# Kernel optimization log

Hardware: AMD Instinct MI355X
Metric: run time of the kernel (lower is better)

## Reference

```python
import jax, jax.numpy as jnp
import numpy as np

DIM = 256
BETA = 4
B, L, L1 = 16, 2048, 4096
EPS = 1e-6


def setup_inputs() -> dict:
    key = jax.random.key(0)
    ks = jax.random.split(key, 20)
    d, db = DIM, DIM // BETA
    s = lambda *sh: 0.02
    inp = {
        "features": jax.random.normal(ks[0], (B, L, d), jnp.float32),
        "quires_box": jax.random.uniform(ks[1], (B, L1, 2), jnp.float32),
        "quires_features": jax.random.normal(ks[2], (B, L1, d), jnp.float32),
        "pos_feature": jax.random.normal(ks[3], (B, L1, d), jnp.float32),
        # contrast1 params
        "c1_w1": jax.random.normal(ks[4], (db, d), jnp.float32) * 0.02,
        "c1_b1": jnp.zeros((db,), jnp.float32),
        "c1_w2": jax.random.normal(ks[5], (d, db), jnp.float32) * 0.02,
        "c1_b2": jnp.zeros((d,), jnp.float32),
        "c1_g": jnp.ones((d,), jnp.float32),
        "c1_be": jnp.zeros((d,), jnp.float32),
        # contrast2 params
        "c2_w1": jax.random.normal(ks[6], (db, d), jnp.float32) * 0.02,
        "c2_b1": jnp.zeros((db,), jnp.float32),
        "c2_w2": jax.random.normal(ks[7], (d, db), jnp.float32) * 0.02,
        "c2_b2": jnp.zeros((d,), jnp.float32),
        "c2_g": jnp.ones((d,), jnp.float32),
        "c2_be": jnp.zeros((d,), jnp.float32),
        # gate MLP (Prediction: Linear(2d->d)+ReLU+Linear(d->2), dropout=identity at eval)
        "g_w1": jax.random.normal(ks[8], (d, 2 * d), jnp.float32) * 0.02,
        "g_b1": jnp.zeros((d,), jnp.float32),
        "g_w2": jax.random.normal(ks[9], (2, d), jnp.float32) * 0.02,
        "g_b2": jnp.zeros((2,), jnp.float32),
    }
    return inp


def _contrast(v1, v2, w1, b1, w2, b2, g, be):
    # v1, v2: [B, N, C]. Pointwise conv1 -> ReLU -> conv2 -> LayerNorm -> sigmoid -> *v1
    v = v1 * v2
    h = jax.nn.relu(jnp.einsum('bnc,dc->bnd', v, w1) + b1)  # [B,N,C/beta]
    u = jnp.einsum('bnd,cd->bnc', h, w2) + b2               # [B,N,C]
    mu = jnp.mean(u, axis=-1, keepdims=True)
    var = jnp.mean(jnp.square(u - mu), axis=-1, keepdims=True)
    ln = (u - mu) * jax.lax.rsqrt(var + EPS) * g + be
    return jax.nn.sigmoid(ln) * v1


def reference(features, quires_box, quires_features, pos_feature,
              c1_w1, c1_b1, c1_w2, c1_b2, c1_g, c1_be,
              c2_w1, c2_b1, c2_w2, c2_b2, c2_g, c2_be,
              g_w1, g_b1, g_w2, g_b2):
    Lf = features.shape[1]
    cx, w = quires_box[..., 0], quires_box[..., 1]
    roi_start = jnp.round(jnp.clip((cx - w / 2) * Lf, 0, Lf - 1)).astype(jnp.int32)
    roi_end = jnp.round(jnp.clip((cx + w / 2) * Lf, 0, Lf - 1)).astype(jnp.int32)
    sf = jnp.take_along_axis(features, roi_start[..., None], axis=1)  # [B,L1,C]
    ef = jnp.take_along_axis(features, roi_end[..., None], axis=1)    # [B,L1,C]
    sf = _contrast(sf, pos_feature, c1_w1, c1_b1, c1_w2, c1_b2, c1_g, c1_be)
    ef = _contrast(ef, pos_feature, c2_w1, c2_b1, c2_w2, c2_b2, c2_g, c2_be)
    pooled = (sf + ef) * 0.5  # aligned_len=True -> mean over the 2 boundaries
    x = jnp.concatenate([pooled, quires_features], axis=-1)  # [B,L1,2C]
    h = jax.nn.relu(jnp.einsum('bnc,dc->bnd', x, g_w1) + g_b1)
    gate = jax.nn.softmax(jnp.einsum('bnd,od->bno', h, g_w2) + g_b2, axis=-1)
    out = pooled * gate[..., 0:1] + quires_features * gate[..., 1:2]
    return jnp.swapaxes(out, 0, 1)  # [L1, B, C]
```

## Files before the change

kernel.cpp:

```cpp
#include <hip/hip_runtime.h>
#include <hip/hip_bf16.h>
#include <math.h>

typedef __attribute__((ext_vector_type(8))) short bf16x8;
typedef __attribute__((ext_vector_type(4))) float f32x4;
typedef __attribute__((ext_vector_type(2))) __fp16 f16x2;
typedef __attribute__((ext_vector_type(4))) unsigned int u32x4;
typedef __attribute__((ext_vector_type(2))) unsigned int u32x2;

constexpr int NB = 16, NQ = 4096, LF = 2048, C = 256;

__device__ __forceinline__ unsigned short bfbits(float x) {
    return __builtin_bit_cast(unsigned short, __float2bfloat16(x));
}
__device__ __forceinline__ unsigned pk2(float a, float b) {
    return (unsigned)bfbits(a) | ((unsigned)bfbits(b) << 16);
}
__device__ __forceinline__ float bflo(unsigned d) { return __builtin_bit_cast(float, d << 16); }
__device__ __forceinline__ float bfhi(unsigned d) { return __builtin_bit_cast(float, d & 0xffff0000u); }
__device__ __forceinline__ unsigned pkh(float a, float b) {
    f16x2 h = __builtin_amdgcn_cvt_pkrtz(a, b);
    return __builtin_bit_cast(unsigned, h);
}
__device__ __forceinline__ float hlo(unsigned u) {
    f16x2 h = __builtin_bit_cast(f16x2, u); return (float)h[0];
}
__device__ __forceinline__ float hhi(unsigned u) {
    f16x2 h = __builtin_bit_cast(f16x2, u); return (float)h[1];
}

__global__ void prep_weights(const float* __restrict__ c1w1, const float* __restrict__ c2w1,
                             const float* __restrict__ c1w2, const float* __restrict__ c2w2,
                             const float* __restrict__ gw1, unsigned short* __restrict__ ws)
{
    int t = blockIdx.x * 256 + threadIdx.x;
    const float* src; int K, nks, dstoff, f;
    if (t < 2048)      { src = c1w1; K = 256; nks = 8;  dstoff = 0;      f = t; }
    else if (t < 4096) { src = c2w1; K = 256; nks = 8;  dstoff = 16384;  f = t - 2048; }
    else if (t < 6144) { src = c1w2; K = 64;  nks = 2;  dstoff = 32768;  f = t - 4096; }
    else if (t < 8192) { src = c2w2; K = 64;  nks = 2;  dstoff = 49152;  f = t - 6144; }
    else               { src = gw1;  K = 512; nks = 16; dstoff = 65536;  f = t - 8192; }
    int l = f & 63, s = f >> 6;
    int nt = s / nks, ks = s % nks;
    int n  = nt * 16 + (l & 15);
    int k0 = ks * 32 + (l >> 4) * 8;
    unsigned short* d = ws + dstoff + (size_t)f * 8;
    const float* sp = src + (size_t)n * K + k0;
    #pragma unroll
    for (int e = 0; e < 8; ++e) d[e] = bfbits(sp[e]);
}

__global__ __launch_bounds__(256, 4)
void semalign_v17(const float* __restrict__ feat,  const float* __restrict__ qbox,
                  const float* __restrict__ qfeat, const float* __restrict__ posf,
                  const float* __restrict__ c1b1,  const float* __restrict__ c1b2,
                  const float* __restrict__ c1g,   const float* __restrict__ c1be,
                  const float* __restrict__ c2b1,  const float* __restrict__ c2b2,
                  const float* __restrict__ c2g,   const float* __restrict__ c2be,
                  const float* __restrict__ gb1,   const float* __restrict__ gw2,
                  const float* __restrict__ gb2,
                  const unsigned short* __restrict__ wsb,
                  float* __restrict__ out)
{
    __shared__ __align__(16) unsigned short sP[4][16][256];

    const int tid = threadIdx.x, l = tid & 63, wid = tid >> 6;
    const int lr = l & 15, lg = l >> 4;
    const int rowb = blockIdx.x * 64 + wid * 16;
    const int q = rowb >> 4;
    const int b = lr;
    const int swz = (lr & 7) << 4;

    const float* prow = posf  + ((size_t)b * NQ + q) * C;
    const float* qrow = qfeat + ((size_t)b * NQ + q) * C;
    float cx = qbox[((size_t)b * NQ + q) * 2 + 0];
    float w  = qbox[((size_t)b * NQ + q) * 2 + 1];
    float fs = fminf(fmaxf((cx - 0.5f * w) * (float)LF, 0.f), (float)(LF - 1));
    float fe = fminf(fmaxf((cx + 0.5f * w) * (float)LF, 0.f), (float)(LF - 1));
    const float* srow = feat + ((size_t)b * LF + (int)rintf(fs)) * C;
    const float* erow = feat + ((size_t)b * LF + (int)rintf(fe)) * C;

    char* pb = (char*)&sP[wid][0][0];
    {
        f32x4 a1[4] = {}, a2[4] = {};
        #pragma unroll
        for (int ks = 0; ks < 8; ++ks) {
            int k0 = ks * 32 + lg * 8;
            float4 s0 = *(const float4*)(srow + k0), s1 = *(const float4*)(srow + k0 + 4);
            float4 e0 = *(const float4*)(erow + k0), e1 = *(const float4*)(erow + k0 + 4);
            float4 p0 = *(const float4*)(prow + k0), p1 = *(const float4*)(prow + k0 + 4);
            u32x4 av, cv;
            av[0] = pk2(s0.x * p0.x, s0.y * p0.y); av[1] = pk2(s0.z * p0.z, s0.w * p0.w);
            av[2] = pk2(s1.x * p1.x, s1.y * p1.y); av[3] = pk2(s1.z * p1.z, s1.w * p1.w);
            cv[0] = pk2(e0.x * p0.x, e0.y * p0.y); cv[1] = pk2(e0.z * p0.z, e0.w * p0.w);
            cv[2] = pk2(e1.x * p1.x, e1.y * p1.y); cv[3] = pk2(e1.z * p1.z, e1.w * p1.w);
            bf16x8 v1 = __builtin_bit_cast(bf16x8, av);
            bf16x8 v2 = __builtin_bit_cast(bf16x8, cv);
            #pragma unroll
            for (int nt = 0; nt < 4; ++nt) {
                bf16x8 wA = *(const bf16x8*)(wsb + ((size_t)((nt * 8 + ks) * 64 + l)) * 8);
                bf16x8 wB = *(const bf16x8*)(wsb + 16384 + ((size_t)((nt * 8 + ks) * 64 + l)) * 8);
                a1[nt] = __builtin_amdgcn_mfma_f32_16x16x32_bf16(wA, v1, a1[nt], 0, 0, 0);
                a2[nt] = __builtin_amdgcn_mfma_f32_16x16x32_bf16(wB, v2, a2[nt], 0, 0, 0);
            }
        }
        #pragma unroll
        for (int nt = 0; nt < 4; ++nt) {
            float4 b1v = *(const float4*)(c1b1 + nt * 16 + lg * 4);
            float4 b2v = *(const float4*)(c2b1 + nt * 16 + lg * 4);
            u32x2 wv;
            wv[0] = pk2(fmaxf(a1[nt][0] + b1v.x, 0.f), fmaxf(a1[nt][1] + b1v.y, 0.f));
            wv[1] = pk2(fmaxf(a1[nt][2] + b1v.z, 0.f), fmaxf(a1[nt][3] + b1v.w, 0.f));
            *(u32x2*)(pb + lr * 128 + ((nt * 32 + lg * 8) ^ swz)) = wv;
            wv[0] = pk2(fmaxf(a2[nt][0] + b2v.x, 0.f), fmaxf(a2[nt][1] + b2v.y, 0.f));
            wv[1] = pk2(fmaxf(a2[nt][2] + b2v.z, 0.f), fmaxf(a2[nt][3] + b2v.w, 0.f));
            *(u32x2*)(pb + 2048 + lr * 128 + ((nt * 32 + lg * 8) ^ swz)) = wv;
        }
    }

    f16x2 Ph[16][2];
    #pragma unroll
    for (int j = 0; j < 2; ++j) {
        char* hb = pb + j * 2048;
        asm volatile("s_waitcnt lgkmcnt(0)" ::: "memory");
        bf16x8 hf0 = *(const bf16x8*)(hb + lr * 128 + ((0 + lg * 16) ^ swz));
        bf16x8 hf1 = *(const bf16x8*)(hb + lr * 128 + ((64 + lg * 16) ^ swz));
        const unsigned short* w2b = wsb + (j ? 49152 : 32768);
        const float* b2p = j ? c2b2 : c1b2;
        const float* gp  = j ? c2g  : c1g;
        const float* bep = j ? c2be : c1be;
        const float* xrow = j ? erow : srow;
        float S = 0.f, Q2 = 0.f;

        {
            f32x4 u8[8] = {};
            #pragma unroll
            for (int nt = 0; nt < 8; ++nt) {
                bf16x8 wA = *(const bf16x8*)(w2b + ((size_t)((nt * 2 + 0) * 64 + l)) * 8);
                bf16x8 wB = *(const bf16x8*)(w2b + ((size_t)((nt * 2 + 1) * 64 + l)) * 8);
                u8[nt] = __builtin_amdgcn_mfma_f32_16x16x32_bf16(wA, hf0, u8[nt], 0, 0, 0);
                u8[nt] = __builtin_amdgcn_mfma_f32_16x16x32_bf16(wB, hf1, u8[nt], 0, 0, 0);
            }
            #pragma unroll
            for (int nt = 0; nt < 8; ++nt) {
                float4 bv = *(const float4*)(b2p + nt * 16 + lg * 4);
                u8[nt][0] += bv.x; u8[nt][1] += bv.y; u8[nt][2] += bv.z; u8[nt][3] += bv.w;
                S  += u8[nt][0] + u8[nt][1] + u8[nt][2] + u8[nt][3];
                Q2 += u8[nt][0] * u8[nt][0] + u8[nt][1] * u8[nt][1]
                    + u8[nt][2] * u8[nt][2] + u8[nt][3] * u8[nt][3];
                u32x2 wv;
                wv[0] = pkh(u8[nt][0], u8[nt][1]);
                wv[1] = pkh(u8[nt][2], u8[nt][3]);
                *(u32x2*)(pb + 4096 + nt * 512 + l * 8) = wv;
            }
        }
        f32x4 u8b[8] = {};
        #pragma unroll
        for (int nt = 0; nt < 8; ++nt) {
            bf16x8 wA = *(const bf16x8*)(w2b + ((size_t)(((nt + 8) * 2 + 0) * 64 + l)) * 8);
            bf16x8 wB = *(const bf16x8*)(w2b + ((size_t)(((nt + 8) * 2 + 1) * 64 + l)) * 8);
            u8b[nt] = __builtin_amdgcn_mfma_f32_16x16x32_bf16(wA, hf0, u8b[nt], 0, 0, 0);
            u8b[nt] = __builtin_amdgcn_mfma_f32_16x16x32_bf16(wB, hf1, u8b[nt], 0, 0, 0);
        }
        #pragma unroll
        for (int nt = 0; nt < 8; ++nt) {
            float4 bv = *(const float4*)(b2p + (nt + 8) * 16 + lg * 4);
            u8b[nt][0] += bv.x; u8b[nt][1] += bv.y; u8b[nt][2] += bv.z; u8b[nt][3] += bv.w;
            S  += u8b[nt][0] + u8b[nt][1] + u8b[nt][2] + u8b[nt][3];
            Q2 += u8b[nt][0] * u8b[nt][0] + u8b[nt][1] * u8b[nt][1]
                + u8b[nt][2] * u8b[nt][2] + u8b[nt][3] * u8b[nt][3];
        }
        S  += __shfl_xor(S, 16);  S  += __shfl_xor(S, 32);
        Q2 += __shfl_xor(Q2, 16); Q2 += __shfl_xor(Q2, 32);
        float mu  = S * (1.f / 256.f);
        float rsg = rsqrtf(Q2 * (1.f / 256.f) - mu * mu + 1e-6f);

        u32x2 st[8];
        asm volatile("s_waitcnt lgkmcnt(0)" ::: "memory");
        #pragma unroll
        for (int nt = 0; nt < 8; ++nt)
            st[nt] = *(const u32x2*)(pb + 4096 + nt * 512 + l * 8);
        asm volatile("s_waitcnt lgkmcnt(0)" ::: "memory");

        #pragma unroll
        for (int nt = 0; nt < 16; ++nt) {
            float u4[4];
            if (nt < 8) {
                u4[0] = hlo(st[nt][0]); u4[1] = hhi(st[nt][0]);
                u4[2] = hlo(st[nt][1]); u4[3] = hhi(st[nt][1]);
            } else {
                u4[0] = u8b[nt - 8][0]; u4[1] = u8b[nt - 8][1];
                u4[2] = u8b[nt - 8][2]; u4[3] = u8b[nt - 8][3];
            }
            float4 gv  = *(const float4*)(gp  + nt * 16 + lg * 4);
            float4 bev = *(const float4*)(bep + nt * 16 + lg * 4);
            float4 xv  = *(const float4*)(xrow + nt * 16 + lg * 4);
            float g4[4] = { gv.x, gv.y, gv.z, gv.w };
            float e4[4] = { bev.x, bev.y, bev.z, bev.w };
            float x4[4] = { xv.x, xv.y, xv.z, xv.w };
            float tm[4];
            #pragma unroll
            for (int r = 0; r < 4; ++r) {
                float ln = (u4[r] - mu) * rsg * g4[r] + e4[r];
                float sg = 1.f / (1.f + __expf(-ln));
                tm[r] = 0.5f * sg * x4[r];
            }
            if (j == 0) {
                Ph[nt][0] = __builtin_amdgcn_cvt_pkrtz(tm[0], tm[1]);
                Ph[nt][1] = __builtin_amdgcn_cvt_pkrtz(tm[2], tm[3]);
            } else {
                float p0 = (float)Ph[nt][0][0] + tm[0];
                float p1 = (float)Ph[nt][0][1] + tm[1];
                float p2 = (float)Ph[nt][1][0] + tm[2];
                float p3 = (float)Ph[nt][1][1] + tm[3];
                u32x2 wv;
                wv[0] = pk2(p0, p1); wv[1] = pk2(p2, p3);
                *(u32x2*)(pb + lr * 512 + ((nt * 32 + lg * 8) ^ swz)) = wv;
            }
        }
    }
    asm volatile("s_waitcnt lgkmcnt(0)" ::: "memory");

    f32x4 ga[16] = {};
    const unsigned short* gwb = wsb + 65536;
    #pragma clang loop unroll(disable)
    for (int kk = 0; kk < 16; ++kk) {
        bf16x8 xk;
        if (kk < 8) {
            xk = *(const bf16x8*)(pb + lr * 512 + ((kk * 64 + lg * 16) ^ swz));
        } else {
            int k0 = (kk - 8) * 32 + lg * 8;
            float4 q0 = *(const float4*)(qrow + k0), q1 = *(const float4*)(qrow + k0 + 4);
            u32x4 a;
            a[0] = pk2(q0.x, q0.y); a[1] = pk2(q0.z, q0.w);
            a[2] = pk2(q1.x, q1.y); a[3] = pk2(q1.z, q1.w);
            xk = __builtin_bit_cast(bf16x8, a);
        }
        #pragma unroll
        for (int nt = 0; nt < 16; ++nt) {
            bf16x8 wf = *(const bf16x8*)(gwb + ((size_t)((nt * 16 + kk) * 64 + l)) * 8);
            ga[nt] = __builtin_amdgcn_mfma_f32_16x16x32_bf16(wf, xk, ga[nt], 0, 0, 0);
        }
    }

    float t0 = 0.f, t1 = 0.f;
    #pragma unroll
    for (int nt = 0; nt < 16; ++nt) {
        float4 gbv = *(const float4*)(gb1 + nt * 16 + lg * 4);
        float4 w0v = *(const float4*)(gw2 + nt * 16 + lg * 4);
        float4 w1v = *(const float4*)(gw2 + 256 + nt * 16 + lg * 4);
        float gb4[4] = { gbv.x, gbv.y, gbv.z, gbv.w };
        float w04[4] = { w0v.x, w0v.y, w0v.z, w0v.w };
        float w14[4] = { w1v.x, w1v.y, w1v.z, w1v.w };
        #pragma unroll
        for (int r = 0; r < 4; ++r) {
            float hv = fmaxf(ga[nt][r] + gb4[r], 0.f);
            t0 += hv * w04[r]; t1 += hv * w14[r];
        }
    }
    t0 += __shfl_xor(t0, 16); t0 += __shfl_xor(t0, 32);
    t1 += __shfl_xor(t1, 16); t1 += __shfl_xor(t1, 32);
    float g0 = 1.f / (1.f + __expf((t1 + gb2[1]) - (t0 + gb2[0])));
    float g1 = 1.f - g0;

    float* orow = out + (size_t)(rowb + lr) * C;
    #pragma unroll
    for (int ks = 0; ks < 8; ++ks) {
        bf16x8 pf = *(const bf16x8*)(pb + lr * 512 + ((ks * 64 + lg * 16) ^ swz));
        u32x4 pu = __builtin_bit_cast(u32x4, pf);
        int k0 = ks * 32 + lg * 8;
        float4 q0 = *(const float4*)(qrow + k0), q1 = *(const float4*)(qrow + k0 + 4);
        float4 o0, o1;
        o0.x = bflo(pu[0]) * g0 + q0.x * g1;
        o0.y = bfhi(pu[0]) * g0 + q0.y * g1;
        o0.z = bflo(pu[1]) * g0 + q0.z * g1;
        o0.w = bfhi(pu[1]) * g0 + q0.w * g1;
        o1.x = bflo(pu[2]) * g0 + q1.x * g1;
        o1.y = bfhi(pu[2]) * g0 + q1.y * g1;
        o1.z = bflo(pu[3]) * g0 + q1.z * g1;
        o1.w = bfhi(pu[3]) * g0 + q1.w * g1;
        *(float4*)(orow + ks * 32 + lg * 8)     = o0;
        *(float4*)(orow + ks * 32 + lg * 8 + 4) = o1;
    }
}

extern "C" void kernel_launch(void* const* d_in, const int* in_sizes, int n_in,
                              void* d_out, int out_size, void* d_ws, size_t ws_size,
                              hipStream_t stream) {
    const float* feat  = (const float*)d_in[0];
    const float* qbox  = (const float*)d_in[1];
    const float* qfeat = (const float*)d_in[2];
    const float* posf  = (const float*)d_in[3];
    const float* c1w1  = (const float*)d_in[4];
    const float* c1b1  = (const float*)d_in[5];
    const float* c1w2  = (const float*)d_in[6];
    const float* c1b2  = (const float*)d_in[7];
    const float* c1g   = (const float*)d_in[8];
    const float* c1be  = (const float*)d_in[9];
    const float* c2w1  = (const float*)d_in[10];
    const float* c2b1  = (const float*)d_in[11];
    const float* c2w2  = (const float*)d_in[12];
    const float* c2b2  = (const float*)d_in[13];
    const float* c2g   = (const float*)d_in[14];
    const float* c2be  = (const float*)d_in[15];
    const float* gw1   = (const float*)d_in[16];
    const float* gb1   = (const float*)d_in[17];
    const float* gw2   = (const float*)d_in[18];
    const float* gb2   = (const float*)d_in[19];
    float* out = (float*)d_out;
    unsigned short* wsb = (unsigned short*)d_ws;

    prep_weights<<<96, 256, 0, stream>>>(c1w1, c2w1, c1w2, c2w2, gw1, wsb);

    dim3 grid((NB * NQ) / 64), block(256);
    semalign_v17<<<grid, block, 0, stream>>>(
        feat, qbox, qfeat, posf,
        c1b1, c1b2, c1g, c1be,
        c2b1, c2b2, c2g, c2be,
        gb1, gw2, gb2, wsb, out);
}
```

Measured before the change: 162.8 us.

## Recompute second-layer contrast MFMAs instead of staging u through LDS and registers

```diff
diff --git a/kernel.cpp b/kernel.cpp
--- a/kernel.cpp
+++ b/kernel.cpp
@@ -4,7 +4,6 @@
 
 typedef __attribute__((ext_vector_type(8))) short bf16x8;
 typedef __attribute__((ext_vector_type(4))) float f32x4;
-typedef __attribute__((ext_vector_type(2))) __fp16 f16x2;
 typedef __attribute__((ext_vector_type(4))) unsigned int u32x4;
 typedef __attribute__((ext_vector_type(2))) unsigned int u32x2;
 
@@ -18,16 +17,6 @@
 }
 __device__ __forceinline__ float bflo(unsigned d) { return __builtin_bit_cast(float, d << 16); }
 __device__ __forceinline__ float bfhi(unsigned d) { return __builtin_bit_cast(float, d & 0xffff0000u); }
-__device__ __forceinline__ unsigned pkh(float a, float b) {
-    f16x2 h = __builtin_amdgcn_cvt_pkrtz(a, b);
-    return __builtin_bit_cast(unsigned, h);
-}
-__device__ __forceinline__ float hlo(unsigned u) {
-    f16x2 h = __builtin_bit_cast(f16x2, u); return (float)h[0];
-}
-__device__ __forceinline__ float hhi(unsigned u) {
-    f16x2 h = __builtin_bit_cast(f16x2, u); return (float)h[1];
-}
 
 __global__ void prep_weights(const float* __restrict__ c1w1, const float* __restrict__ c2w1,
                              const float* __restrict__ c1w2, const float* __restrict__ c2w2,
@@ -51,7 +40,7 @@
 }
 
 __global__ __launch_bounds__(256, 4)
-void semalign_v17(const float* __restrict__ feat,  const float* __restrict__ qbox,
+void semalign_v18(const float* __restrict__ feat,  const float* __restrict__ qbox,
                   const float* __restrict__ qfeat, const float* __restrict__ posf,
                   const float* __restrict__ c1b1,  const float* __restrict__ c1b2,
                   const float* __restrict__ c1g,   const float* __restrict__ c1be,
@@ -118,105 +107,92 @@
         }
     }
 
-    f16x2 Ph[16][2];
+    asm volatile("s_waitcnt lgkmcnt(0)" ::: "memory");
+    bf16x8 hfA0 = *(const bf16x8*)(pb + lr * 128 + ((0  + lg * 16) ^ swz));
+    bf16x8 hfA1 = *(const bf16x8*)(pb + lr * 128 + ((64 + lg * 16) ^ swz));
+    bf16x8 hfB0 = *(const bf16x8*)(pb + 2048 + lr * 128 + ((0  + lg * 16) ^ swz));
+    bf16x8 hfB1 = *(const bf16x8*)(pb + 2048 + lr * 128 + ((64 + lg * 16) ^ swz));
+    asm volatile("s_waitcnt lgkmcnt(0)" ::: "memory");
+
+    float S1 = 0.f, Q21 = 0.f, S2 = 0.f, Q22 = 0.f;
     #pragma unroll
     for (int j = 0; j < 2; ++j) {
-        char* hb = pb + j * 2048;
-        asm volatile("s_waitcnt lgkmcnt(0)" ::: "memory");
-        bf16x8 hf0 = *(const bf16x8*)(hb + lr * 128 + ((0 + lg * 16) ^ swz));
-        bf16x8 hf1 = *(const bf16x8*)(hb + lr * 128 + ((64 + lg * 16) ^ swz));
         const unsigned short* w2b = wsb + (j ? 49152 : 32768);
         const float* b2p = j ? c2b2 : c1b2;
-        const float* gp  = j ? c2g  : c1g;
-        const float* bep = j ? c2be : c1be;
-        const float* xrow = j ? erow : srow;
+        bf16x8 h0 = j ? hfB0 : hfA0, h1 = j ? hfB1 : hfA1;
         float S = 0.f, Q2 = 0.f;
-
+        #pragma unroll
+        for (int nt = 0; nt < 16; ++nt) {
+            f32x4 u = {};
+            bf16x8 wA = *(const bf16x8*)(w2b + ((size_t)((nt * 2 + 0) * 64 + l)) * 8);
+            bf16x8 wB = *(const bf16x8*)(w2b + ((size_t)((nt * 2 + 1) * 64 + l)) * 8);
+            u = __builtin_amdgcn_mfma_f32_16x16x32_bf16(wA, h0, u, 0, 0, 0);
+            u = __builtin_amdgcn_mfma_f32_16x16x32_bf16(wB, h1, u, 0, 0, 0);
+            float4 bv = *(const float4*)(b2p + nt * 16 + lg * 4);
+            float b4[4] = { bv.x, bv.y, bv.z, bv.w };
+            #pragma unroll
+            for (int r = 0; r < 4; ++r) {
+                float v = u[r] + b4[r];
+                S += v; Q2 += v * v;
+            }
+        }
+        if (j == 0) { S1 = S; Q21 = Q2; } else { S2 = S; Q22 = Q2; }
+    }
+    S1 += __shfl_xor(S1, 16); S1 += __shfl_xor(S1, 32);
+    Q21 += __shfl_xor(Q21, 16); Q21 += __shfl_xor(Q21, 32);
+    S2 += __shfl_xor(S2, 16); S2 += __shfl_xor(S2, 32);
+    Q22 += __shfl_xor(Q22, 16); Q22 += __shfl_xor(Q22, 32);
+    float mu1 = S1 * (1.f / 256.f), rs1 = rsqrtf(Q21 * (1.f / 256.f) - mu1 * mu1 + 1e-6f);
+    float mu2 = S2 * (1.f / 256.f), rs2 = rsqrtf(Q22 * (1.f / 256.f) - mu2 * mu2 + 1e-6f);
+
+    #pragma unroll
+    for (int nt = 0; nt < 16; ++nt) {
+        float tm[4];
         {
-            f32x4 u8[8] = {};
-            #pragma unroll
-            for (int nt = 0; nt < 8; ++nt) {
-                bf16x8 wA = *(const bf16x8*)(w2b + ((size_t)((nt * 2 + 0) * 64 + l)) * 8);
-                bf16x8 wB = *(const bf16x8*)(w2b + ((size_t)((nt * 2 + 1) * 64 + l)) * 8);
-                u8[nt] = __builtin_amdgcn_mfma_f32_16x16x32_bf16(wA, hf0, u8[nt], 0, 0, 0);
-                u8[nt] = __builtin_amdgcn_mfma_f32_16x16x32_bf16(wB, hf1, u8[nt], 0, 0, 0);
-            }
-            #pragma unroll
-            for (int nt = 0; nt < 8; ++nt) {
-                float4 bv = *(const float4*)(b2p + nt * 16 + lg * 4);
-                u8[nt][0] += bv.x; u8[nt][1] += bv.y; u8[nt][2] += bv.z; u8[nt][3] += bv.w;
-                S  += u8[nt][0] + u8[nt][1] + u8[nt][2] + u8[nt][3];
-                Q2 += u8[nt][0] * u8[nt][0] + u8[nt][1] * u8[nt][1]
-                    + u8[nt][2] * u8[nt][2] + u8[nt][3] * u8[nt][3];
-                u32x2 wv;
-                wv[0] = pkh(u8[nt][0], u8[nt][1]);
-                wv[1] = pkh(u8[nt][2], u8[nt][3]);
-                *(u32x2*)(pb + 4096 + nt * 512 + l * 8) = wv;
-            }
-        }
-        f32x4 u8b[8] = {};
-        #pragma unroll
-        for (int nt = 0; nt < 8; ++nt) {
-            bf16x8 wA = *(const bf16x8*)(w2b + ((size_t)(((nt + 8) * 2 + 0) * 64 + l)) * 8);
-            bf16x8 wB = *(const bf16x8*)(w2b + ((size_t)(((nt + 8) * 2 + 1) * 64 + l)) * 8);
-            u8b[nt] = __builtin_amdgcn_mfma_f32_16x16x32_bf16(wA, hf0, u8b[nt], 0, 0, 0);
-            u8b[nt] = __builtin_amdgcn_mfma_f32_16x16x32_bf16(wB, hf1, u8b[nt], 0, 0, 0);
-        }
-        #pragma unroll
-        for (int nt = 0; nt < 8; ++nt) {
-            float4 bv = *(const float4*)(b2p + (nt + 8) * 16 + lg * 4);
-            u8b[nt][0] += bv.x; u8b[nt][1] += bv.y; u8b[nt][2] += bv.z; u8b[nt][3] += bv.w;
-            S  += u8b[nt][0] + u8b[nt][1] + u8b[nt][2] + u8b[nt][3];
-            Q2 += u8b[nt][0] * u8b[nt][0] + u8b[nt][1] * u8b[nt][1]
-                + u8b[nt][2] * u8b[nt][2] + u8b[nt][3] * u8b[nt][3];
-        }
-        S  += __shfl_xor(S, 16);  S  += __shfl_xor(S, 32);
-        Q2 += __shfl_xor(Q2, 16); Q2 += __shfl_xor(Q2, 32);
-        float mu  = S * (1.f / 256.f);
-        float rsg = rsqrtf(Q2 * (1.f / 256.f) - mu * mu + 1e-6f);
-
-        u32x2 st[8];
-        asm volatile("s_waitcnt lgkmcnt(0)" ::: "memory");
-        #pragma unroll
-        for (int nt = 0; nt < 8; ++nt)
-            st[nt] = *(const u32x2*)(pb + 4096 + nt * 512 + l * 8);
-        asm volatile("s_waitcnt lgkmcnt(0)" ::: "memory");
-
-        #pragma unroll
-        for (int nt = 0; nt < 16; ++nt) {
-            float u4[4];
-            if (nt < 8) {
-                u4[0] = hlo(st[nt][0]); u4[1] = hhi(st[nt][0]);
-                u4[2] = hlo(st[nt][1]); u4[3] = hhi(st[nt][1]);
-            } else {
-                u4[0] = u8b[nt - 8][0]; u4[1] = u8b[nt - 8][1];
-                u4[2] = u8b[nt - 8][2]; u4[3] = u8b[nt - 8][3];
-            }
-            float4 gv  = *(const float4*)(gp  + nt * 16 + lg * 4);
-            float4 bev = *(const float4*)(bep + nt * 16 + lg * 4);
-            float4 xv  = *(const float4*)(xrow + nt * 16 + lg * 4);
+            f32x4 u = {};
+            bf16x8 wA = *(const bf16x8*)(wsb + 32768 + ((size_t)((nt * 2 + 0) * 64 + l)) * 8);
+            bf16x8 wB = *(const bf16x8*)(wsb + 32768 + ((size_t)((nt * 2 + 1) * 64 + l)) * 8);
+            u = __builtin_amdgcn_mfma_f32_16x16x32_bf16(wA, hfA0, u, 0, 0, 0);
+            u = __builtin_amdgcn_mfma_f32_16x16x32_bf16(wB, hfA1, u, 0, 0, 0);
+            float4 bv = *(const float4*)(c1b2 + nt * 16 + lg * 4);
+            float4 gv = *(const float4*)(c1g  + nt * 16 + lg * 4);
+            float4 ev = *(const float4*)(c1be + nt * 16 + lg * 4);
+            float4 xv = *(const float4*)(srow + nt * 16 + lg * 4);
+            float b4[4] = { bv.x, bv.y, bv.z, bv.w };
             float g4[4] = { gv.x, gv.y, gv.z, gv.w };
-            float e4[4] = { bev.x, bev.y, bev.z, bev.w };
+            float e4[4] = { ev.x, ev.y, ev.z, ev.w };
             float x4[4] = { xv.x, xv.y, xv.z, xv.w };
-            float tm[4];
             #pragma unroll
             for (int r = 0; r < 4; ++r) {
-                float ln = (u4[r] - mu) * rsg * g4[r] + e4[r];
+                float ln = (u[r] + b4[r] - mu1) * rs1 * g4[r] + e4[r];
                 float sg = 1.f / (1.f + __expf(-ln));
                 tm[r] = 0.5f * sg * x4[r];
             }
-            if (j == 0) {
-                Ph[nt][0] = __builtin_amdgcn_cvt_pkrtz(tm[0], tm[1]);
-                Ph[nt][1] = __builtin_amdgcn_cvt_pkrtz(tm[2], tm[3]);
-            } else {
-                float p0 = (float)Ph[nt][0][0] + tm[0];
-                float p1 = (float)Ph[nt][0][1] + tm[1];
-                float p2 = (float)Ph[nt][1][0] + tm[2];
-                float p3 = (float)Ph[nt][1][1] + tm[3];
-                u32x2 wv;
-                wv[0] = pk2(p0, p1); wv[1] = pk2(p2, p3);
-                *(u32x2*)(pb + lr * 512 + ((nt * 32 + lg * 8) ^ swz)) = wv;
-            }
+        }
+        {
+            f32x4 u = {};
+            bf16x8 wA = *(const bf16x8*)(wsb + 49152 + ((size_t)((nt * 2 + 0) * 64 + l)) * 8);
+            bf16x8 wB = *(const bf16x8*)(wsb + 49152 + ((size_t)((nt * 2 + 1) * 64 + l)) * 8);
+            u = __builtin_amdgcn_mfma_f32_16x16x32_bf16(wA, hfB0, u, 0, 0, 0);
+            u = __builtin_amdgcn_mfma_f32_16x16x32_bf16(wB, hfB1, u, 0, 0, 0);
+            float4 bv = *(const float4*)(c2b2 + nt * 16 + lg * 4);
+            float4 gv = *(const float4*)(c2g  + nt * 16 + lg * 4);
+            float4 ev = *(const float4*)(c2be + nt * 16 + lg * 4);
+            float4 xv = *(const float4*)(erow + nt * 16 + lg * 4);
+            float b4[4] = { bv.x, bv.y, bv.z, bv.w };
+            float g4[4] = { gv.x, gv.y, gv.z, gv.w };
+            float e4[4] = { ev.x, ev.y, ev.z, ev.w };
+            float x4[4] = { xv.x, xv.y, xv.z, xv.w };
+            float pm[4];
+            #pragma unroll
+            for (int r = 0; r < 4; ++r) {
+                float ln = (u[r] + b4[r] - mu2) * rs2 * g4[r] + e4[r];
+                float sg = 1.f / (1.f + __expf(-ln));
+                pm[r] = tm[r] + 0.5f * sg * x4[r];
+            }
+            u32x2 wv;
+            wv[0] = pk2(pm[0], pm[1]); wv[1] = pk2(pm[2], pm[3]);
+            *(u32x2*)(pb + lr * 512 + ((nt * 32 + lg * 8) ^ swz)) = wv;
         }
     }
     asm volatile("s_waitcnt lgkmcnt(0)" ::: "memory");
@@ -313,7 +289,7 @@
     prep_weights<<<96, 256, 0, stream>>>(c1w1, c2w1, c1w2, c2w2, gw1, wsb);
 
     dim3 grid((NB * NQ) / 64), block(256);
-    semalign_v17<<<grid, block, 0, stream>>>(
+    semalign_v18<<<grid, block, 0, stream>>>(
         feat, qbox, qfeat, posf,
         c1b1, c1b2, c1g, c1be,
         c2b1, c2b2, c2g, c2be,
```

After: 242.8 us. 49.1% more time.
